# Kernel optimization log

Measured on AMD Instinct MI355X. Metric: run time of the kernel, lower is better.

Reference implementation:

```python
import jax, jax.numpy as jnp
import numpy as np

# config constants (match init_kwargs)
EPS = 1e-6
LAYER_TEMP = 1.0
MIN_GATE = 0.1
MAX_GATE = 0.9
MAX_STATE_NORM = 10.0
EVIDENCE_SCALE = 256.0
STATE_DECAY = 0.0

B, L, E, H, G, R = 2, 32, 256, 4096, 16, 64


def _normalize(x, axis=-1):
    # torch F.normalize: x / max(||x||, eps)
    n = jnp.linalg.norm(x, axis=axis, keepdims=True)
    return x / jnp.maximum(n, EPS)


def setup_inputs() -> dict:
    key = jax.random.key(0)
    ks = jax.random.split(key, 8)
    return {
        "state": jax.random.normal(ks[0], (B, R), jnp.float32),
        "evicted_k": jax.random.normal(ks[1], (B, L, E, H), jnp.float32) * 0.02,
        "evicted_v": jax.random.normal(ks[2], (B, L, E, H), jnp.float32) * 0.02,
        "Wq": jax.random.normal(ks[3], (R, H), jnp.float32) * 0.02,
        "Wk": jax.random.normal(ks[4], (R, H), jnp.float32) * 0.02,
        "Wv": jax.random.normal(ks[5], (R, H), jnp.float32) * 0.02,
        "global_q": jax.random.normal(ks[6], (G, H), jnp.float32) * 0.02,
        "layer_query": jax.random.normal(ks[7], (R,), jnp.float32) * 0.02,
        "evicted_tokens_per_layer": 256,
    }


def reference(state, evicted_k, evicted_v, Wq, Wk, Wv, global_q, layer_query,
              evicted_tokens_per_layer):
    rank = Wq.shape[0]
    inv_sqrt_r = 1.0 / jnp.sqrt(jnp.float32(rank))

    # ---- layer attention over L (use_layer_attention=True) ----
    layer_k = evicted_k.mean(axis=2)                                  # [B,L,H]
    layer_scores = jnp.einsum('blh,rh,r->bl', layer_k, Wk, layer_query)
    layer_scores = layer_scores * (inv_sqrt_r / LAYER_TEMP)
    layer_w = jax.nn.softmax(layer_scores, axis=1)                    # [B,L]
    ek = jnp.einsum('bleh,bl->beh', evicted_k, layer_w)               # [B,E,H]
    ev = jnp.einsum('bleh,bl->beh', evicted_v, layer_w)               # [B,E,H]

    # ---- low-rank cross attention: global queries over evicted tokens ----
    q = global_q @ Wq.T                                               # [G,R]
    k = jnp.einsum('beh,rh->ber', ek, Wk)                             # [B,E,R]
    v = jnp.einsum('beh,rh->ber', ev, Wv)                             # [B,E,R]
    scores = jnp.einsum('gr,ber->bge', q, k) * inv_sqrt_r             # [B,G,E]
    attn = jax.nn.softmax(scores, axis=-1)
    context = jnp.einsum('bge,ber->bgr', attn, v)                     # [B,G,R]
    s_new = context.mean(axis=1)                                      # [B,R]

    # ---- gated state update (detach_prev_state=True) ----
    prev = jax.lax.stop_gradient(state)
    sim = jnp.sum(_normalize(prev) * _normalize(s_new), axis=-1)
    sim = jnp.clip(sim, -1.0, 1.0)
    gate = MIN_GATE + (MAX_GATE - MIN_GATE) * 0.5 * (sim + 1.0)
    evidence = jnp.minimum(1.0, jnp.float32(evicted_tokens_per_layer) / EVIDENCE_SCALE)
    gate = (gate * evidence)[:, None]                                 # [B,1]

    updated = (1.0 - STATE_DECAY) * (1.0 - gate) * prev + gate * s_new

    # clamp state norm to max_state_norm
    n = jnp.linalg.norm(updated, axis=-1, keepdims=True)
    updated = updated * jnp.minimum(1.0, MAX_STATE_NORM / jnp.maximum(n, EPS))
    return updated
```

## Files before the change

### kernel.cpp

```cpp
#include <hip/hip_runtime.h>
#include <hip/hip_bf16.h>
#include <stdint.h>

#define BB 2
#define LL 32
#define EE 256
#define HH 4096
#define GG 16
#define RR 64

typedef __bf16 bf16x8 __attribute__((ext_vector_type(8)));
typedef float f32x4 __attribute__((ext_vector_type(4)));

__device__ inline void async16(const void* g, void* l) {
    __builtin_amdgcn_global_load_lds((const __attribute__((address_space(1))) uint32_t*)g,
                                     (__attribute__((address_space(3))) uint32_t*)l, 16, 0, 0);
}

__device__ inline bf16x8 cvt8(f32x4 a, f32x4 b) {
    bf16x8 r;
    r[0] = (__bf16)a[0]; r[1] = (__bf16)a[1]; r[2] = (__bf16)a[2]; r[3] = (__bf16)a[3];
    r[4] = (__bf16)b[0]; r[5] = (__bf16)b[1]; r[6] = (__bf16)b[2]; r[7] = (__bf16)b[3];
    return r;
}

__global__ __launch_bounds__(256) void prep_kernel(
    const float* __restrict__ Wk, const float* __restrict__ Wv,
    __hip_bfloat16* __restrict__ Bfrag, float* __restrict__ scores)
{
    const int tid = blockIdx.x * 256 + threadIdx.x;
    const int mat = tid >> 15;
    const int r   = (tid >> 9) & 63;
    const int kq  = tid & 511;
    const float* W = mat ? Wv : Wk;
    const float* src = W + (size_t)r * HH + kq * 8;
    f32x4 a = *(const f32x4*)src;
    f32x4 b = *(const f32x4*)(src + 4);
    bf16x8 o = cvt8(a, b);
    *(bf16x8*)((__bf16*)Bfrag + ((size_t)(mat * 512 + kq) * 64 + r) * 8) = o;
    if (blockIdx.x == 0 && threadIdx.x < BB * LL) scores[threadIdx.x] = 0.f;
}

__global__ __launch_bounds__(256) void proj_kernel(
    const float* __restrict__ ek, const float* __restrict__ ev,
    const __hip_bfloat16* __restrict__ Bfrag, const float* __restrict__ lq,
    __hip_bfloat16* __restrict__ kpart, __hip_bfloat16* __restrict__ vpart,
    float* __restrict__ scores)
{
    __shared__ __align__(16) float smem[16640];
    uint8_t* sm = (uint8_t*)smem;

    const int blk  = blockIdx.x;
    const int bl   = blk >> 3;
    const int e0   = (blk & 7) * 32;
    const int t    = threadIdx.x;
    const int w    = t >> 6;
    const int lane = t & 63;
    const int n    = lane & 15;
    const int quad = lane >> 4;

    const int mat = w >> 1;
    const int mt  = w & 1;

    f32x4 acc[4] = {};
    const size_t rowbase = (size_t)bl * EE + e0;

    const float* asrc = (w == 0) ? ek : ev;
    const float* agp0 = asrc + (rowbase + (lane >> 5)) * (size_t)HH + (lane & 31) * 4;
    const __hip_bfloat16* bsrc = Bfrag + (size_t)(w & 1) * 512 * 64 * 8;
    uint8_t* adst = sm + w * 16896;
    uint8_t* bdst = sm + 33792 + (w & 1) * 16384;

    const uint8_t* abase = sm + mat * 16896;
    const uint8_t* bbase = sm + 33792 + mat * 16384;
    const int m = mt * 16 + n;
    const uint8_t* arow = abase + (m >> 1) * 1056 + (m & 1) * 512;

    for (int c = 0; c < 32; c++) {
        const int h0 = c * 128;
        if (w < 2) {
            const float* gp = agp0 + h0;
#pragma unroll
            for (int p = 0; p < 16; p++)
                async16(gp + (size_t)2 * p * HH, adst + p * 1056);
        } else {
            const __hip_bfloat16* gp = bsrc + ((size_t)(c * 16) * 64 + lane) * 8;
#pragma unroll
            for (int kq = 0; kq < 16; kq++)
                async16(gp + (size_t)kq * 64 * 8, bdst + kq * 1024);
        }
        __syncthreads();
#pragma unroll
        for (int kc = 0; kc < 4; kc++) {
            const float* ap = (const float*)(arow + (kc * 32 + quad * 8) * 4);
            f32x4 a0 = *(const f32x4*)ap;
            f32x4 a1 = *(const f32x4*)(ap + 4);
            bf16x8 af = cvt8(a0, a1);
#pragma unroll
            for (int nt = 0; nt < 4; nt++) {
                bf16x8 bfv = *(const bf16x8*)(bbase + (size_t)((kc * 4 + quad) * 64 + nt * 16 + n) * 16);
                acc[nt] = __builtin_amdgcn_mfma_f32_16x16x32_bf16(af, bfv, acc[nt], 0, 0, 0);
            }
        }
        __syncthreads();
    }

    __hip_bfloat16* outp = (mat == 0) ? kpart : vpart;
    float lqv[4];
    if (mat == 0) {
#pragma unroll
        for (int nt = 0; nt < 4; nt++) lqv[nt] = lq[nt * 16 + n];
    }
    float sc = 0.f;
#pragma unroll
    for (int nt = 0; nt < 4; nt++)
#pragma unroll
        for (int reg = 0; reg < 4; reg++) {
            const int e_row = e0 + mt * 16 + quad * 4 + reg;
            outp[((size_t)bl * EE + e_row) * RR + nt * 16 + n] = __float2bfloat16(acc[nt][reg]);
            if (mat == 0) sc += acc[nt][reg] * lqv[nt];
        }
    if (mat == 0) {
#pragma unroll
        for (int off = 32; off > 0; off >>= 1) sc += __shfl_down(sc, off, 64);
        if (lane == 0) atomicAdd(&scores[bl], sc);
    }
}

__global__ __launch_bounds__(256) void kber_kernel(
    const __hip_bfloat16* __restrict__ kpart, const __hip_bfloat16* __restrict__ vpart,
    const float* __restrict__ scores,
    float* __restrict__ kberT, float* __restrict__ vberT)
{
    const int blk = blockIdx.x;
    const int b   = blk >> 3;
    const int e0  = (blk & 7) * 32;
    const int t   = threadIdx.x;
    __shared__ float wl[LL];
    if (t == 0) {
        float s[LL]; float mx = -1e30f;
        for (int l = 0; l < LL; l++) { s[l] = scores[b * LL + l] * (1.f / 2048.f); mx = fmaxf(mx, s[l]); }
        float sum = 0.f;
        for (int l = 0; l < LL; l++) { s[l] = __expf(s[l] - mx); sum += s[l]; }
        const float inv = 1.0f / sum;
        for (int l = 0; l < LL; l++) wl[l] = s[l] * inv;
    }
    __syncthreads();
    const int e_l = t >> 3;
    const int r0  = (t & 7) * 8;
    float sk[8] = {}, sv[8] = {};
    for (int l = 0; l < LL; l++) {
        const float wv_ = wl[l];
        const size_t base = ((size_t)(b * LL + l) * EE + e0 + e_l) * RR + r0;
        bf16x8 k8 = *(const bf16x8*)((const __bf16*)kpart + base);
        bf16x8 v8 = *(const bf16x8*)((const __bf16*)vpart + base);
#pragma unroll
        for (int j = 0; j < 8; j++) { sk[j] += wv_ * (float)k8[j]; sv[j] += wv_ * (float)v8[j]; }
    }
    const int e = e0 + e_l;
#pragma unroll
    for (int j = 0; j < 8; j++) {
        kberT[((size_t)b * RR + r0 + j) * EE + e] = sk[j];
        vberT[((size_t)b * RR + r0 + j) * EE + e] = sv[j];
    }
}

__global__ __launch_bounds__(256) void qproj_kernel(
    const float* __restrict__ gq, const float* __restrict__ Wq,
    float* __restrict__ q)
{
    const int g  = blockIdx.x >> 2;
    const int rq = blockIdx.x & 3;
    const int t  = threadIdx.x;
    __shared__ float red[16][256];
    __shared__ float r2[16][17];
    float s[16] = {};
    for (int i = 0; i < 4; i++) {
        const int h = i * 1024 + t * 4;
        f32x4 a = *(const f32x4*)(gq + (size_t)g * HH + h);
#pragma unroll
        for (int r = 0; r < 16; r++) {
            f32x4 wv_ = *(const f32x4*)(Wq + (size_t)(rq * 16 + r) * HH + h);
            s[r] += a[0] * wv_[0] + a[1] * wv_[1] + a[2] * wv_[2] + a[3] * wv_[3];
        }
    }
#pragma unroll
    for (int r = 0; r < 16; r++) red[r][t] = s[r];
    __syncthreads();
    {
        const int r = t >> 4, j = t & 15;
        float p = 0.f;
        for (int i = 0; i < 16; i++) p += red[r][j * 16 + i];
        r2[r][j] = p;
    }
    __syncthreads();
    if (t < 16) {
        float p = 0.f;
        for (int j = 0; j < 16; j++) p += r2[t][j];
        q[g * RR + rq * 16 + t] = p;
    }
}

__global__ __launch_bounds__(256) void final_kernel(
    const float* __restrict__ q, const float* __restrict__ kberT,
    const float* __restrict__ vberT, const float* __restrict__ state,
    const int* __restrict__ tokens, float* __restrict__ out)
{
    const int b = blockIdx.x;
    const int t = threadIdx.x;
    __shared__ float qs[GG * RR];
    __shared__ float red[256];
    __shared__ float p[EE];
    __shared__ float ctx2[RR][5];
    __shared__ float sacc[RR];
    __shared__ float prevs[RR], news[RR], upd[RR];
    __shared__ float gate_s, scale_s;

    for (int i = t; i < GG * RR; i += 256) qs[i] = q[i];
    if (t < RR) sacc[t] = 0.f;
    __syncthreads();

    const float* kT = kberT + (size_t)b * RR * EE;
    const float* vT = vberT + (size_t)b * RR * EE;

    for (int g = 0; g < GG; g++) {
        float s = 0.f;
#pragma unroll 8
        for (int r = 0; r < RR; r++) s += qs[g * RR + r] * kT[(size_t)r * EE + t];
        s *= 0.125f;
        red[t] = s; __syncthreads();
        for (int off = 128; off > 0; off >>= 1) {
            if (t < off) red[t] = fmaxf(red[t], red[t + off]);
            __syncthreads();
        }
        const float mx = red[0];
        __syncthreads();
        const float ex = __expf(s - mx);
        red[t] = ex; __syncthreads();
        for (int off = 128; off > 0; off >>= 1) {
            if (t < off) red[t] += red[t + off];
            __syncthreads();
        }
        const float inv = 1.0f / red[0];
        __syncthreads();
        p[t] = ex * inv;
        __syncthreads();
        const int r  = t >> 2;
        const int es = t & 3;
        const float* vrow = vT + (size_t)r * EE + es * 64;
        float c = 0.f;
#pragma unroll 4
        for (int i = 0; i < 64; i++) c += p[es * 64 + i] * vrow[i];
        ctx2[r][es] = c;
        __syncthreads();
        if (t < RR) sacc[t] += (ctx2[t][0] + ctx2[t][1] + ctx2[t][2] + ctx2[t][3]) * (1.0f / GG);
        __syncthreads();
    }

    if (t < RR) { prevs[t] = state[b * RR + t]; news[t] = sacc[t]; }
    __syncthreads();
    if (t == 0) {
        float np = 0.f, ns = 0.f, dp = 0.f;
        for (int r = 0; r < RR; r++) {
            np += prevs[r] * prevs[r];
            ns += news[r] * news[r];
            dp += prevs[r] * news[r];
        }
        np = sqrtf(np); ns = sqrtf(ns);
        float sim = dp / (fmaxf(np, 1e-6f) * fmaxf(ns, 1e-6f));
        sim = fminf(1.0f, fmaxf(-1.0f, sim));
        float gate = 0.1f + 0.8f * 0.5f * (sim + 1.0f);
        const int tv = tokens[0];
        float tokf;
        if (tv >= 0 && tv < (1 << 24)) tokf = (float)tv;
        else tokf = __int_as_float(tv);
        const float evidence = fminf(1.0f, tokf * (1.0f / 256.0f));
        gate_s = gate * evidence;
    }
    __syncthreads();
    const float gate = gate_s;
    if (t < RR) upd[t] = (1.0f - gate) * prevs[t] + gate * news[t];
    __syncthreads();
    if (t == 0) {
        float nn = 0.f;
        for (int r = 0; r < RR; r++) nn += upd[r] * upd[r];
        nn = sqrtf(nn);
        scale_s = fminf(1.0f, 10.0f / fmaxf(nn, 1e-6f));
    }
    __syncthreads();
    if (t < RR) out[b * RR + t] = upd[t] * scale_s;
}

extern "C" void kernel_launch(void* const* d_in, const int* in_sizes, int n_in,
                              void* d_out, int out_size, void* d_ws, size_t ws_size,
                              hipStream_t stream) {
    const float* state = (const float*)d_in[0];
    const float* ek    = (const float*)d_in[1];
    const float* ev    = (const float*)d_in[2];
    const float* Wq    = (const float*)d_in[3];
    const float* Wk    = (const float*)d_in[4];
    const float* Wv    = (const float*)d_in[5];
    const float* gq    = (const float*)d_in[6];
    const float* lq    = (const float*)d_in[7];
    const int*   tok   = (const int*)d_in[8];
    float* out = (float*)d_out;

    const size_t n_part = (size_t)BB * LL * EE * RR;
    __hip_bfloat16* kpart = (__hip_bfloat16*)d_ws;
    __hip_bfloat16* vpart = kpart + n_part;
    __hip_bfloat16* Bfrag = vpart + n_part;
    float* fr      = (float*)(Bfrag + (size_t)2 * 512 * 64 * 8);
    float* scores  = fr;
    float* kberT   = scores + BB * LL;
    float* vberT   = kberT + (size_t)BB * RR * EE;
    float* qbuf    = vberT + (size_t)BB * RR * EE;

    prep_kernel<<<256, 256, 0, stream>>>(Wk, Wv, Bfrag, scores);
    proj_kernel<<<512, 256, 0, stream>>>(ek, ev, Bfrag, lq, kpart, vpart, scores);
    kber_kernel<<<16, 256, 0, stream>>>(kpart, vpart, scores, kberT, vberT);
    qproj_kernel<<<64, 256, 0, stream>>>(gq, Wq, qbuf);
    final_kernel<<<BB, 256, 0, stream>>>(qbuf, kberT, vberT, state, tok, out);
}
```

Baseline: 633.2 us.

## Triple-buffer projection GEMM with swizzled LDS and rewrite reduction kernels with shuffles

The projection kernel now uses a three-stage async-to-LDS pipeline with smaller 32-wide K chunks, XOR-swizzled A rows to avoid bank conflicts, a single barrier per iteration, and a 4-blocks-per-SM launch bound to improve occupancy. The Wk/Wv repack writes contiguously. The kber kernel is split per matrix with a wave-shuffle softmax and a row-major output, and the final kernel drops its many block-level barrier reductions for per-wave shuffle reductions over groups of queries. Together these aim to overlap the memory stream that dominates the runtime and to cut synchronisation overhead. In exchange the pipelining relies on hand-written waitcnt counts, which makes correctness fragile.

```diff
diff --git a/kernel.cpp b/kernel.cpp
--- a/kernel.cpp
+++ b/kernel.cpp
@@ -30,25 +30,25 @@
 {
     const int tid = blockIdx.x * 256 + threadIdx.x;
     const int mat = tid >> 15;
-    const int r   = (tid >> 9) & 63;
-    const int kq  = tid & 511;
+    const int kq  = (tid >> 6) & 511;
+    const int r   = tid & 63;
     const float* W = mat ? Wv : Wk;
     const float* src = W + (size_t)r * HH + kq * 8;
     f32x4 a = *(const f32x4*)src;
     f32x4 b = *(const f32x4*)(src + 4);
-    bf16x8 o = cvt8(a, b);
-    *(bf16x8*)((__bf16*)Bfrag + ((size_t)(mat * 512 + kq) * 64 + r) * 8) = o;
+    *(bf16x8*)((__bf16*)Bfrag + (size_t)tid * 8) = cvt8(a, b);
     if (blockIdx.x == 0 && threadIdx.x < BB * LL) scores[threadIdx.x] = 0.f;
 }
 
-__global__ __launch_bounds__(256) void proj_kernel(
+__global__ __launch_bounds__(256, 4) void proj_kernel(
     const float* __restrict__ ek, const float* __restrict__ ev,
     const __hip_bfloat16* __restrict__ Bfrag, const float* __restrict__ lq,
     __hip_bfloat16* __restrict__ kpart, __hip_bfloat16* __restrict__ vpart,
     float* __restrict__ scores)
 {
-    __shared__ __align__(16) float smem[16640];
-    uint8_t* sm = (uint8_t*)smem;
+    __shared__ __align__(16) uint8_t sm[49152];
+    uint8_t* smA = sm;
+    uint8_t* smB = sm + 24576;
 
     const int blk  = blockIdx.x;
     const int bl   = blk >> 3;
@@ -57,66 +57,80 @@
     const int w    = t >> 6;
     const int lane = t & 63;
     const int n    = lane & 15;
-    const int quad = lane >> 4;
-
-    const int mat = w >> 1;
-    const int mt  = w & 1;
+    const int q    = lane >> 4;
+    const int mat  = w >> 1;
+    const int mt   = w & 1;
+
+    const int row_l = lane >> 3;
+    const int aswz  = ((lane & 7) ^ row_l) << 4;
+    const char* astage = (const char*)((w & 1) ? ev : ek)
+        + ((size_t)(bl * EE + e0 + row_l) * HH) * 4 + aswz;
+    const char* bstage = (const char*)Bfrag + ((w & 1) ? (size_t)512 * 1024 : (size_t)0)
+        + (size_t)lane * 16;
+    uint8_t* adst0 = smA + (w & 1) * 4096;
+    uint8_t* bdst0 = smB + (w & 1) * 4096;
+    const bool isA = (w < 2);
+
+    auto stage = [&](int cc, int sb) {
+        if (isA) {
+            const char* g = astage + (size_t)cc * 128;
+            uint8_t* d = adst0 + sb * 8192;
+#pragma unroll
+            for (int p = 0; p < 4; ++p)
+                async16(g + (size_t)p * (8 * HH * 4), d + p * 1024);
+        } else {
+            const char* g = bstage + (size_t)cc * 4096;
+            uint8_t* d = bdst0 + sb * 8192;
+#pragma unroll
+            for (int i = 0; i < 4; ++i)
+                async16(g + i * 1024, d + i * 1024);
+        }
+    };
 
     f32x4 acc[4] = {};
-    const size_t rowbase = (size_t)bl * EE + e0;
-
-    const float* asrc = (w == 0) ? ek : ev;
-    const float* agp0 = asrc + (rowbase + (lane >> 5)) * (size_t)HH + (lane & 31) * 4;
-    const __hip_bfloat16* bsrc = Bfrag + (size_t)(w & 1) * 512 * 64 * 8;
-    uint8_t* adst = sm + w * 16896;
-    uint8_t* bdst = sm + 33792 + (w & 1) * 16384;
-
-    const uint8_t* abase = sm + mat * 16896;
-    const uint8_t* bbase = sm + 33792 + mat * 16384;
     const int m = mt * 16 + n;
-    const uint8_t* arow = abase + (m >> 1) * 1056 + (m & 1) * 512;
-
-    for (int c = 0; c < 32; c++) {
-        const int h0 = c * 128;
-        if (w < 2) {
-            const float* gp = agp0 + h0;
-#pragma unroll
-            for (int p = 0; p < 16; p++)
-                async16(gp + (size_t)2 * p * HH, adst + p * 1056);
-        } else {
-            const __hip_bfloat16* gp = bsrc + ((size_t)(c * 16) * 64 + lane) * 8;
-#pragma unroll
-            for (int kq = 0; kq < 16; kq++)
-                async16(gp + (size_t)kq * 64 * 8, bdst + kq * 1024);
-        }
-        __syncthreads();
-#pragma unroll
-        for (int kc = 0; kc < 4; kc++) {
-            const float* ap = (const float*)(arow + (kc * 32 + quad * 8) * 4);
-            f32x4 a0 = *(const f32x4*)ap;
-            f32x4 a1 = *(const f32x4*)(ap + 4);
-            bf16x8 af = cvt8(a0, a1);
-#pragma unroll
-            for (int nt = 0; nt < 4; nt++) {
-                bf16x8 bfv = *(const bf16x8*)(bbase + (size_t)((kc * 4 + quad) * 64 + nt * 16 + n) * 16);
-                acc[nt] = __builtin_amdgcn_mfma_f32_16x16x32_bf16(af, bfv, acc[nt], 0, 0, 0);
-            }
-        }
-        __syncthreads();
+    const uint8_t* arow0 = smA + mat * 4096 + m * 128;
+    const int sA0 = ((2 * q) ^ (n & 7)) << 4;
+    const int sA1 = ((2 * q + 1) ^ (n & 7)) << 4;
+    const uint8_t* brow0 = smB + mat * 4096 + q * 1024 + n * 16;
+
+    stage(0, 0);
+    stage(1, 1);
+
+    int cb = 0;
+    for (int c = 0; c < 128; ++c) {
+        asm volatile("s_waitcnt vmcnt(4)" ::: "memory");
+        __builtin_amdgcn_s_barrier();
+        asm volatile("" ::: "memory");
+
+        stage((c + 2) & 127, cb >= 1 ? cb - 1 : 2);
+
+        const uint8_t* arow = arow0 + cb * 8192;
+        f32x4 a0 = *(const f32x4*)(arow + sA0);
+        f32x4 a1 = *(const f32x4*)(arow + sA1);
+        bf16x8 af = cvt8(a0, a1);
+        const uint8_t* brow = brow0 + cb * 8192;
+#pragma unroll
+        for (int nt = 0; nt < 4; ++nt) {
+            bf16x8 bv = *(const bf16x8*)(brow + nt * 256);
+            acc[nt] = __builtin_amdgcn_mfma_f32_16x16x32_bf16(af, bv, acc[nt], 0, 0, 0);
+        }
+        asm volatile("" ::: "memory");
+        cb = (cb == 2) ? 0 : cb + 1;
     }
 
     __hip_bfloat16* outp = (mat == 0) ? kpart : vpart;
     float lqv[4];
     if (mat == 0) {
 #pragma unroll
-        for (int nt = 0; nt < 4; nt++) lqv[nt] = lq[nt * 16 + n];
+        for (int nt = 0; nt < 4; ++nt) lqv[nt] = lq[nt * 16 + n];
     }
     float sc = 0.f;
 #pragma unroll
-    for (int nt = 0; nt < 4; nt++)
-#pragma unroll
-        for (int reg = 0; reg < 4; reg++) {
-            const int e_row = e0 + mt * 16 + quad * 4 + reg;
+    for (int nt = 0; nt < 4; ++nt)
+#pragma unroll
+        for (int reg = 0; reg < 4; ++reg) {
+            const int e_row = e0 + mt * 16 + q * 4 + reg;
             outp[((size_t)bl * EE + e_row) * RR + nt * 16 + n] = __float2bfloat16(acc[nt][reg]);
             if (mat == 0) sc += acc[nt][reg] * lqv[nt];
         }
@@ -125,44 +139,45 @@
         for (int off = 32; off > 0; off >>= 1) sc += __shfl_down(sc, off, 64);
         if (lane == 0) atomicAdd(&scores[bl], sc);
     }
+    asm volatile("s_waitcnt vmcnt(0)" ::: "memory");
 }
 
 __global__ __launch_bounds__(256) void kber_kernel(
     const __hip_bfloat16* __restrict__ kpart, const __hip_bfloat16* __restrict__ vpart,
     const float* __restrict__ scores,
-    float* __restrict__ kberT, float* __restrict__ vberT)
+    float* __restrict__ k2, float* __restrict__ v2)
 {
     const int blk = blockIdx.x;
-    const int b   = blk >> 3;
+    const int b   = blk >> 4;
+    const int mat = (blk >> 3) & 1;
     const int e0  = (blk & 7) * 32;
-    const int t   = threadIdx.x;
-    __shared__ float wl[LL];
-    if (t == 0) {
-        float s[LL]; float mx = -1e30f;
-        for (int l = 0; l < LL; l++) { s[l] = scores[b * LL + l] * (1.f / 2048.f); mx = fmaxf(mx, s[l]); }
-        float sum = 0.f;
-        for (int l = 0; l < LL; l++) { s[l] = __expf(s[l] - mx); sum += s[l]; }
-        const float inv = 1.0f / sum;
-        for (int l = 0; l < LL; l++) wl[l] = s[l] * inv;
-    }
-    __syncthreads();
-    const int e_l = t >> 3;
-    const int r0  = (t & 7) * 8;
-    float sk[8] = {}, sv[8] = {};
-    for (int l = 0; l < LL; l++) {
-        const float wv_ = wl[l];
-        const size_t base = ((size_t)(b * LL + l) * EE + e0 + e_l) * RR + r0;
-        bf16x8 k8 = *(const bf16x8*)((const __bf16*)kpart + base);
-        bf16x8 v8 = *(const bf16x8*)((const __bf16*)vpart + base);
-#pragma unroll
-        for (int j = 0; j < 8; j++) { sk[j] += wv_ * (float)k8[j]; sv[j] += wv_ * (float)v8[j]; }
-    }
-    const int e = e0 + e_l;
-#pragma unroll
-    for (int j = 0; j < 8; j++) {
-        kberT[((size_t)b * RR + r0 + j) * EE + e] = sk[j];
-        vberT[((size_t)b * RR + r0 + j) * EE + e] = sv[j];
-    }
+    const int t = threadIdx.x, w = t >> 6, lane = t & 63;
+
+    float sv = scores[b * LL + (lane & 31)] * (1.f / 2048.f);
+    float mx = sv;
+#pragma unroll
+    for (int off = 16; off; off >>= 1) mx = fmaxf(mx, __shfl_xor(mx, off));
+    float ex = __expf(sv - mx), sum = ex;
+#pragma unroll
+    for (int off = 16; off; off >>= 1) sum += __shfl_xor(sum, off);
+    const float wgt = ex / sum;
+
+    const int e  = e0 + w * 8 + (lane >> 3);
+    const int r8 = (lane & 7) * 8;
+    const __hip_bfloat16* src = mat ? vpart : kpart;
+    const __bf16* base = (const __bf16*)src + ((size_t)b * LL * EE + e) * RR + r8;
+    float acc[8] = {};
+    for (int l = 0; l < LL; ++l) {
+        const float wl = __shfl(wgt, l);
+        bf16x8 v8 = *(const bf16x8*)(base + (size_t)l * EE * RR);
+#pragma unroll
+        for (int j = 0; j < 8; ++j) acc[j] += wl * (float)v8[j];
+    }
+    float* dst = (mat ? v2 : k2) + ((size_t)b * EE + e) * RR + r8;
+    f32x4 o0 = {acc[0], acc[1], acc[2], acc[3]};
+    f32x4 o1 = {acc[4], acc[5], acc[6], acc[7]};
+    *(f32x4*)dst = o0;
+    *(f32x4*)(dst + 4) = o1;
 }
 
 __global__ __launch_bounds__(256) void qproj_kernel(
@@ -202,93 +217,85 @@
 }
 
 __global__ __launch_bounds__(256) void final_kernel(
-    const float* __restrict__ q, const float* __restrict__ kberT,
-    const float* __restrict__ vberT, const float* __restrict__ state,
+    const float* __restrict__ q, const float* __restrict__ k2,
+    const float* __restrict__ v2, const float* __restrict__ state,
     const int* __restrict__ tokens, float* __restrict__ out)
 {
     const int b = blockIdx.x;
     const int t = threadIdx.x;
+    const int w = t >> 6, lane = t & 63;
     __shared__ float qs[GG * RR];
-    __shared__ float red[256];
-    __shared__ float p[EE];
-    __shared__ float ctx2[RR][5];
-    __shared__ float sacc[RR];
-    __shared__ float prevs[RR], news[RR], upd[RR];
-    __shared__ float gate_s, scale_s;
+    __shared__ float ctxw[4][RR];
 
     for (int i = t; i < GG * RR; i += 256) qs[i] = q[i];
-    if (t < RR) sacc[t] = 0.f;
     __syncthreads();
 
-    const float* kT = kberT + (size_t)b * RR * EE;
-    const float* vT = vberT + (size_t)b * RR * EE;
-
-    for (int g = 0; g < GG; g++) {
-        float s = 0.f;
+    const float* kb = k2 + (size_t)b * EE * RR;
+    const float* vb = v2 + (size_t)b * EE * RR;
+    float ctxsum = 0.f;
+#pragma unroll
+    for (int gi = 0; gi < 4; ++gi) {
+        const int g = w * 4 + gi;
+        float sarr[4];
+#pragma unroll
+        for (int k = 0; k < 4; ++k) {
+            const float* krow = kb + (size_t)(k * 64 + lane) * RR;
+            f32x4 a = {};
+#pragma unroll
+            for (int r4 = 0; r4 < 16; ++r4) {
+                f32x4 kv = *(const f32x4*)(krow + r4 * 4);
+                f32x4 qv = *(const f32x4*)(qs + g * RR + r4 * 4);
+                a += kv * qv;
+            }
+            sarr[k] = (a[0] + a[1] + a[2] + a[3]) * 0.125f;
+        }
+        float mx = fmaxf(fmaxf(sarr[0], sarr[1]), fmaxf(sarr[2], sarr[3]));
+#pragma unroll
+        for (int off = 32; off; off >>= 1) mx = fmaxf(mx, __shfl_xor(mx, off));
+        float ps[4]; float sum = 0.f;
+#pragma unroll
+        for (int k = 0; k < 4; ++k) { ps[k] = __expf(sarr[k] - mx); sum += ps[k]; }
+#pragma unroll
+        for (int off = 32; off; off >>= 1) sum += __shfl_xor(sum, off);
+        const float inv = 1.0f / sum;
+        float c = 0.f;
+#pragma unroll
+        for (int k = 0; k < 4; ++k) {
+            const float pk = ps[k] * inv;
 #pragma unroll 8
-        for (int r = 0; r < RR; r++) s += qs[g * RR + r] * kT[(size_t)r * EE + t];
-        s *= 0.125f;
-        red[t] = s; __syncthreads();
-        for (int off = 128; off > 0; off >>= 1) {
-            if (t < off) red[t] = fmaxf(red[t], red[t + off]);
-            __syncthreads();
-        }
-        const float mx = red[0];
-        __syncthreads();
-        const float ex = __expf(s - mx);
-        red[t] = ex; __syncthreads();
-        for (int off = 128; off > 0; off >>= 1) {
-            if (t < off) red[t] += red[t + off];
-            __syncthreads();
-        }
-        const float inv = 1.0f / red[0];
-        __syncthreads();
-        p[t] = ex * inv;
-        __syncthreads();
-        const int r  = t >> 2;
-        const int es = t & 3;
-        const float* vrow = vT + (size_t)r * EE + es * 64;
-        float c = 0.f;
-#pragma unroll 4
-        for (int i = 0; i < 64; i++) c += p[es * 64 + i] * vrow[i];
-        ctx2[r][es] = c;
-        __syncthreads();
-        if (t < RR) sacc[t] += (ctx2[t][0] + ctx2[t][1] + ctx2[t][2] + ctx2[t][3]) * (1.0f / GG);
-        __syncthreads();
-    }
-
-    if (t < RR) { prevs[t] = state[b * RR + t]; news[t] = sacc[t]; }
+            for (int e = 0; e < 64; ++e) {
+                const float pe = __shfl(pk, e);
+                c += pe * vb[(size_t)(k * 64 + e) * RR + lane];
+            }
+        }
+        ctxsum += c;
+    }
+    ctxw[w][lane] = ctxsum;
     __syncthreads();
-    if (t == 0) {
-        float np = 0.f, ns = 0.f, dp = 0.f;
-        for (int r = 0; r < RR; r++) {
-            np += prevs[r] * prevs[r];
-            ns += news[r] * news[r];
-            dp += prevs[r] * news[r];
-        }
-        np = sqrtf(np); ns = sqrtf(ns);
-        float sim = dp / (fmaxf(np, 1e-6f) * fmaxf(ns, 1e-6f));
+
+    if (w == 0) {
+        const float snew = (ctxw[0][lane] + ctxw[1][lane] + ctxw[2][lane] + ctxw[3][lane]) * (1.0f / GG);
+        const float prev = state[b * RR + lane];
+        float np = prev * prev, ns = snew * snew, dp = prev * snew;
+#pragma unroll
+        for (int off = 32; off; off >>= 1) {
+            np += __shfl_xor(np, off);
+            ns += __shfl_xor(ns, off);
+            dp += __shfl_xor(dp, off);
+        }
+        float sim = dp / (fmaxf(sqrtf(np), 1e-6f) * fmaxf(sqrtf(ns), 1e-6f));
         sim = fminf(1.0f, fmaxf(-1.0f, sim));
         float gate = 0.1f + 0.8f * 0.5f * (sim + 1.0f);
         const int tv = tokens[0];
-        float tokf;
-        if (tv >= 0 && tv < (1 << 24)) tokf = (float)tv;
-        else tokf = __int_as_float(tv);
-        const float evidence = fminf(1.0f, tokf * (1.0f / 256.0f));
-        gate_s = gate * evidence;
-    }
-    __syncthreads();
-    const float gate = gate_s;
-    if (t < RR) upd[t] = (1.0f - gate) * prevs[t] + gate * news[t];
-    __syncthreads();
-    if (t == 0) {
-        float nn = 0.f;
-        for (int r = 0; r < RR; r++) nn += upd[r] * upd[r];
-        nn = sqrtf(nn);
-        scale_s = fminf(1.0f, 10.0f / fmaxf(nn, 1e-6f));
-    }
-    __syncthreads();
-    if (t < RR) out[b * RR + t] = upd[t] * scale_s;
+        float tokf = (tv >= 0 && tv < (1 << 24)) ? (float)tv : __int_as_float(tv);
+        gate *= fminf(1.0f, tokf * (1.0f / 256.0f));
+        const float upd = (1.0f - gate) * prev + gate * snew;
+        float nn = upd * upd;
+#pragma unroll
+        for (int off = 32; off; off >>= 1) nn += __shfl_xor(nn, off);
+        const float scale = fminf(1.0f, 10.0f / fmaxf(sqrtf(nn), 1e-6f));
+        out[b * RR + lane] = upd * scale;
+    }
 }
 
 extern "C" void kernel_launch(void* const* d_in, const int* in_sizes, int n_in,
@@ -311,13 +318,13 @@
     __hip_bfloat16* Bfrag = vpart + n_part;
     float* fr      = (float*)(Bfrag + (size_t)2 * 512 * 64 * 8);
     float* scores  = fr;
-    float* kberT   = scores + BB * LL;
-    float* vberT   = kberT + (size_t)BB * RR * EE;
-    float* qbuf    = vberT + (size_t)BB * RR * EE;
+    float* k2      = scores + BB * LL;
+    float* v2      = k2 + (size_t)BB * EE * RR;
+    float* qbuf    = v2 + (size_t)BB * EE * RR;
 
     prep_kernel<<<256, 256, 0, stream>>>(Wk, Wv, Bfrag, scores);
     proj_kernel<<<512, 256, 0, stream>>>(ek, ev, Bfrag, lq, kpart, vpart, scores);
-    kber_kernel<<<16, 256, 0, stream>>>(kpart, vpart, scores, kberT, vberT);
+    kber_kernel<<<32, 256, 0, stream>>>(kpart, vpart, scores, k2, v2);
     qproj_kernel<<<64, 256, 0, stream>>>(gq, Wq, qbuf);
-    final_kernel<<<BB, 256, 0, stream>>>(qbuf, kberT, vberT, state, tok, out);
-}
+    final_kernel<<<BB, 256, 0, stream>>>(qbuf, k2, v2, state, tok, out);
+}
```

New measurement: 616.1 us. -2.7%, faster.
